# Performance work log

Hardware: AMD Instinct MI355X
Metric: run time of the kernel (lower is better)

Reference implementation:

```python
import jax, jax.numpy as jnp
import numpy as np

EPS = 1e-5


def _bn(h, gamma, beta):
    # BatchNorm1d, training mode: biased batch statistics over nodes
    mu = jnp.mean(h, axis=0)
    var = jnp.mean(jnp.square(h - mu), axis=0)
    return (h - mu) * jax.lax.rsqrt(var + EPS) * gamma + beta


def setup_inputs() -> dict:
    key = jax.random.key(0)
    ks = jax.random.split(key, 12)
    N, E, D, H = 50000, 800000, 128, 256
    x = jax.random.normal(ks[0], (N, D), dtype=jnp.float32)
    edge_index = jax.random.randint(ks[1], (2, E), 0, N, dtype=jnp.int64)
    train_node_id = jax.random.randint(ks[2], (10000,), 0, N, dtype=jnp.int64)
    def lin(k, fan_in, fan_out):
        bound = 1.0 / np.sqrt(fan_in)
        return jax.random.uniform(k, (fan_in, fan_out), jnp.float32, -bound, bound)
    return {
        "x": x, "edge_index": edge_index, "train_node_id": train_node_id,
        "W1": lin(ks[3], D, H), "b1": jnp.zeros((H,), jnp.float32),
        "W2": lin(ks[4], H, H), "b2": jnp.zeros((H,), jnp.float32),
        "W3": lin(ks[5], H, H), "b3": jnp.zeros((H,), jnp.float32),
        "g1": jnp.ones((H,), jnp.float32), "be1": jnp.zeros((H,), jnp.float32),
        "g2": jnp.ones((H,), jnp.float32), "be2": jnp.zeros((H,), jnp.float32),
        "g3": jnp.ones((H,), jnp.float32), "be3": jnp.zeros((H,), jnp.float32),
        "Wl": lin(ks[6], H, H), "bl": jnp.zeros((H,), jnp.float32),
        "Wf": lin(ks[7], H, 1), "bf": jnp.zeros((1,), jnp.float32),
    }


def reference(x, edge_index, train_node_id, W1, b1, W2, b2, W3, b3,
              g1, be1, g2, be2, g3, be3, Wl, bl, Wf, bf):
    N = x.shape[0]
    loops = jnp.arange(N, dtype=edge_index.dtype)
    row = jnp.concatenate([edge_index[0], loops])  # destinations
    col = jnp.concatenate([edge_index[1], loops])  # sources
    deg = jax.ops.segment_sum(jnp.ones_like(row, dtype=x.dtype), row, num_segments=N)
    d_isqrt = jax.lax.rsqrt(deg)  # deg >= 1 due to self loops
    norm = (d_isqrt[row] * d_isqrt[col])[:, None]  # [E+N, 1]

    def gcn(h, W, b):
        hW = h @ W
        agg = jax.ops.segment_sum(hW[col] * norm, row, num_segments=N)
        return agg + b

    h = jax.nn.relu(_bn(gcn(x, W1, b1), g1, be1))
    h = jax.nn.relu(_bn(gcn(h, W2, b2), g2, be2))
    h = jax.nn.relu(_bn(gcn(h, W3, b3), g3, be3))
    h = jax.nn.relu(h @ Wl + bl)
    h = h[train_node_id]
    return jnp.squeeze(h @ Wf + bf, -1)
```

## Files before the change

kernel.cpp:

```cpp
#include <hip/hip_runtime.h>

typedef unsigned short u16;
typedef __attribute__((ext_vector_type(8))) short short8;
typedef __attribute__((ext_vector_type(4))) float f32x4;

#define CAP 96

#define DEVFN static __device__ __forceinline__

DEVFN float b2f(u16 u) {
    union { float f; unsigned v; } x; x.v = ((unsigned)u) << 16; return x.f;
}
DEVFN u16 f2b(float f) {
    union { float f; unsigned v; } x; x.f = f;
    unsigned r = x.v + 0x7fffu + ((x.v >> 16) & 1u);
    return (u16)(r >> 16);
}
DEVFN float h2f(u16 u) {
    union { _Float16 h[2]; u16 s[2]; } x; x.s[0] = u; return (float)x.h[0];
}
DEVFN u16 f2h(float f) {
    union { _Float16 h[2]; u16 s[2]; } x; x.h[0] = (_Float16)f; return x.s[0];
}

DEVFN int detect64(const int* __restrict__ p) {
    int orv = 0;
#pragma unroll
    for (int i = 1; i < 64; i += 2) orv |= p[i];
    return (orv == 0) ? 1 : 0;
}

DEVFN void accum_row8(short8 v, float* acc) {
    const unsigned* u = (const unsigned*)&v;
#pragma unroll
    for (int k = 0; k < 4; k++) {
        union { float f; unsigned w; } lo, hi;
        lo.w = u[k] << 16;
        hi.w = u[k] & 0xffff0000u;
        acc[2 * k] += lo.f;
        acc[2 * k + 1] += hi.f;
    }
}

__global__ void k_init(const float* __restrict__ W1, const float* __restrict__ W2,
                       const float* __restrict__ W3, const float* __restrict__ Wl,
                       u16* __restrict__ T1, u16* __restrict__ T2,
                       u16* __restrict__ T3, u16* __restrict__ Tl,
                       int* __restrict__ ssrc, float* __restrict__ stat,
                       float* __restrict__ out, int N, int M) {
    int t = blockIdx.x * 256 + threadIdx.x;
    if (t < 229376) {
        const float* W; u16* T; int K; int idx;
        if (t < 32768)        { W = W1; T = T1; K = 128; idx = t; }
        else if (t < 98304)   { W = W2; T = T2; K = 256; idx = t - 32768; }
        else if (t < 163840)  { W = W3; T = T3; K = 256; idx = t - 98304; }
        else                  { W = Wl; T = Tl; K = 256; idx = t - 163840; }
        int k = idx >> 8, n = idx & 255;
        T[(size_t)n * K + k] = f2b(W[(size_t)k * 256 + n]);
    } else if (t < 229376 + 50000) {
        ssrc[(size_t)(t - 229376) * CAP] = 0;
    } else if (t < 229376 + 50000 + 1536) {
        stat[t - 229376 - 50000] = 0.0f;
    } else if (t < 229376 + 50000 + 1536 + 10000) {
        out[t - 229376 - 50000 - 1536] = 0.0f;
    }
}

__global__ void k_fillb(const int* __restrict__ ei, int* __restrict__ ssrc, int E) {
    int fl = detect64(ei);
    int t = blockIdx.x * 256 + threadIdx.x;
    int e0 = t * 4;
    if (e0 >= E) return;
    int r[4], c[4];
    int nv = min(4, E - e0);
    if (fl) {
        const int4* p4 = (const int4*)ei;
        int4 d0 = p4[2 * t], d1 = p4[2 * t + 1];
        int4 s0 = p4[(E >> 1) + 2 * t], s1 = p4[(E >> 1) + 2 * t + 1];
        r[0] = d0.x; r[1] = d0.z; r[2] = d1.x; r[3] = d1.z;
        c[0] = s0.x; c[1] = s0.z; c[2] = s1.x; c[3] = s1.z;
    } else {
        const int4* p4 = (const int4*)ei;
        int4 d = p4[t];
        int4 s = p4[(E >> 2) + t];
        r[0] = d.x; r[1] = d.y; r[2] = d.z; r[3] = d.w;
        c[0] = s.x; c[1] = s.y; c[2] = s.z; c[3] = s.w;
    }
#pragma unroll
    for (int k = 0; k < 4; k++) {
        if (k < nv) {
            int p = atomicAdd(&ssrc[(size_t)r[k] * CAP], 1);
            if (p < CAP - 1) ssrc[(size_t)r[k] * CAP + 1 + p] = c[k];
        }
    }
}

__global__ void k_cvtx(const float* __restrict__ x, const int* __restrict__ ssrc,
                       float* __restrict__ disq, u16* __restrict__ xb, int n) {
    int i = (blockIdx.x * 256 + threadIdx.x) * 4;
    if (i >= n) return;
    int row = i >> 7;
    float d = rsqrtf((float)(ssrc[(size_t)row * CAP] + 1));
    if ((i & 127) == 0) disq[row] = d;
    float4 v = *(const float4*)(x + i);
    ushort4 o;
    o.x = f2b(v.x * d); o.y = f2b(v.y * d); o.z = f2b(v.z * d); o.w = f2b(v.w * d);
    *(ushort4*)(xb + i) = o;
}


template<int KS>
__global__ __launch_bounds__(256, 2) void k_gemm_rb(
        const u16* __restrict__ A, const u16* __restrict__ Wt, u16* __restrict__ C,
        u16* __restrict__ Ch, const int* __restrict__ idx,
        int Gtot, float* __restrict__ stat, const float* __restrict__ bias, int relu,
        const float* __restrict__ Wfp, const float* __restrict__ bfp,
        float* __restrict__ outp) {
    constexpr int K = KS * 32;
    __shared__ float sbuf[4][2][64];
    int wv = threadIdx.x >> 6;
    int lane = threadIdx.x & 63;
    int quad = lane >> 4;
    int mr = lane & 15;
    int colbase = blockIdx.y * 64;
    int g0 = blockIdx.x * 16;

    short8 Bf[4][KS];
#pragma unroll
    for (int j = 0; j < 4; j++)
#pragma unroll
        for (int s = 0; s < KS; s++)
            Bf[j][s] = *(const short8*)(Wt + (size_t)(colbase + j * 16 + mr) * K + s * 32 + quad * 8);

    float bv[4] = {0.f, 0.f, 0.f, 0.f};
    if (bias) {
#pragma unroll
        for (int j = 0; j < 4; j++) bv[j] = bias[colbase + j * 16 + mr];
    }
    float wf[4] = {0.f, 0.f, 0.f, 0.f};
    if (Wfp) {
#pragma unroll
        for (int j = 0; j < 4; j++) wf[j] = Wfp[colbase + j * 16 + mr];
    }

    float sreg[4] = {0.f, 0.f, 0.f, 0.f};
    float s2reg[4] = {0.f, 0.f, 0.f, 0.f};
    int f = idx ? detect64(idx) : 0;

    for (int g = wv; g < 16; g += 4) {
        int gg = g0 + g;
        if (gg >= Gtot) continue;
        int row = gg * 16 + mr;
        int arow = idx ? idx[(size_t)row << f] : row;
        const u16* Ap = A + (size_t)arow * K + quad * 8;

        short8 Af[KS];
#pragma unroll
        for (int s = 0; s < KS; s++) Af[s] = *(const short8*)(Ap + s * 32);

        f32x4 acc[4];
#pragma unroll
        for (int j = 0; j < 4; j++) acc[j] = (f32x4){0.f, 0.f, 0.f, 0.f};
#pragma unroll
        for (int s = 0; s < KS; s++)
#pragma unroll
            for (int j = 0; j < 4; j++)
                acc[j] = __builtin_amdgcn_mfma_f32_16x16x32_bf16(Af[s], Bf[j][s], acc[j], 0, 0, 0);

        if (Wfp) {
            float partial[4];
#pragma unroll
            for (int r = 0; r < 4; r++) {
                float pr = 0.f;
#pragma unroll
                for (int j = 0; j < 4; j++) {
                    float v = fmaxf(acc[j][r] + bv[j], 0.f);
                    pr += v * wf[j];
                }
                partial[r] = pr;
            }
#pragma unroll
            for (int r = 0; r < 4; r++) {
                partial[r] += __shfl_xor(partial[r], 1, 64);
                partial[r] += __shfl_xor(partial[r], 2, 64);
                partial[r] += __shfl_xor(partial[r], 4, 64);
                partial[r] += __shfl_xor(partial[r], 8, 64);
            }
            if (mr == 0) {
#pragma unroll
                for (int r = 0; r < 4; r++) {
                    int orow = gg * 16 + quad * 4 + r;
                    float v = partial[r];
                    if (blockIdx.y == 0) v += bfp[0];
                    atomicAdd(&outp[orow], v);
                }
            }
            continue;
        }

        size_t cb = (size_t)(gg * 16 + quad * 4) * 256 + colbase + mr;
#pragma unroll
        for (int j = 0; j < 4; j++) {
            float s_ = 0.f, s2_ = 0.f;
#pragma unroll
            for (int r = 0; r < 4; r++) {
                float v = acc[j][r];
                s_ += v; s2_ += v * v;
                if (Ch) {
                    Ch[cb + (size_t)r * 256 + j * 16] = f2h(v);
                } else {
                    v += bv[j];
                    if (relu) v = fmaxf(v, 0.f);
                    C[cb + (size_t)r * 256 + j * 16] = f2b(v);
                }
            }
            sreg[j] += s_;
            s2reg[j] += s2_;
        }
    }

    if (stat) {
#pragma unroll
        for (int j = 0; j < 4; j++) {
            float s_ = sreg[j], s2_ = s2reg[j];
            s_ += __shfl_xor(s_, 16, 64);  s_ += __shfl_xor(s_, 32, 64);
            s2_ += __shfl_xor(s2_, 16, 64); s2_ += __shfl_xor(s2_, 32, 64);
            if (quad == 0) {
                sbuf[wv][0][j * 16 + mr] = s_;
                sbuf[wv][1][j * 16 + mr] = s2_;
            }
        }
        __syncthreads();
        int t = threadIdx.x;
        if (t < 128) {
            int which = t >> 6, c = t & 63;
            float v = sbuf[0][which][c] + sbuf[1][which][c] +
                      sbuf[2][which][c] + sbuf[3][which][c];
            atomicAdd(&stat[which * 256 + colbase + c], v);
        }
    }
}


__global__ __launch_bounds__(256) void k_gather256(
        const u16* __restrict__ src, const int* __restrict__ ssrc,
        const float* __restrict__ disq, u16* __restrict__ dst, int N) {
    int wave = threadIdx.x >> 6;
    int lane = threadIdx.x & 63;
    int half = lane >> 5;
    int l5 = lane & 31;
    int i = blockIdx.x * 4 + wave;
    if (i >= N) return;
    const u16* base = src + l5 * 8;
    const int* sp = ssrc + (size_t)i * CAP;
    float acc[8] = {0.f, 0.f, 0.f, 0.f, 0.f, 0.f, 0.f, 0.f};
    int e = min(sp[0], CAP - 1);
    int p = 0;
    for (; p + 8 <= e; p += 8) {
        int c0 = sp[1 + p + half];
        int c1 = sp[1 + p + 2 + half];
        int c2 = sp[1 + p + 4 + half];
        int c3 = sp[1 + p + 6 + half];
        short8 v0 = *(const short8*)(base + (size_t)c0 * 256);
        short8 v1 = *(const short8*)(base + (size_t)c1 * 256);
        short8 v2 = *(const short8*)(base + (size_t)c2 * 256);
        short8 v3 = *(const short8*)(base + (size_t)c3 * 256);
        accum_row8(v0, acc);
        accum_row8(v1, acc);
        accum_row8(v2, acc);
        accum_row8(v3, acc);
    }
    for (; p + 2 <= e; p += 2) {
        int c = sp[1 + p + half];
        short8 v = *(const short8*)(base + (size_t)c * 256);
        accum_row8(v, acc);
    }
    {
        int c = half ? i : ((p < e) ? sp[1 + p] : -1);
        if (c >= 0) {
            short8 v = *(const short8*)(base + (size_t)c * 256);
            accum_row8(v, acc);
        }
    }
#pragma unroll
    for (int k = 0; k < 8; k++) acc[k] += __shfl_xor(acc[k], 32, 64);
    if (half == 0) {
        float di = disq[i];
        short8 o;
        u16* op = (u16*)&o;
#pragma unroll
        for (int k = 0; k < 8; k++) op[k] = f2b(acc[k] * di);
        *(short8*)(dst + (size_t)i * 256 + l5 * 8) = o;
    }
}

__global__ __launch_bounds__(256) void k_gather128(
        const u16* __restrict__ src, const int* __restrict__ ssrc,
        const float* __restrict__ disq, u16* __restrict__ dst, int N) {
    int wave = threadIdx.x >> 6;
    int lane = threadIdx.x & 63;
    int q = lane >> 4;
    int l4 = lane & 15;
    int i = blockIdx.x * 4 + wave;
    if (i >= N) return;
    const u16* base = src + l4 * 8;
    const int* sp = ssrc + (size_t)i * CAP;
    float acc[8] = {0.f, 0.f, 0.f, 0.f, 0.f, 0.f, 0.f, 0.f};
    int e = min(sp[0], CAP - 1);
    int p = 0;
    for (; p + 8 <= e; p += 8) {
        int c0 = sp[1 + p + q];
        int c1 = sp[1 + p + 4 + q];
        short8 v0 = *(const short8*)(base + (size_t)c0 * 128);
        short8 v1 = *(const short8*)(base + (size_t)c1 * 128);
        accum_row8(v0, acc);
        accum_row8(v1, acc);
    }
    for (; p + 4 <= e; p += 4) {
        int c = sp[1 + p + q];
        short8 v = *(const short8*)(base + (size_t)c * 128);
        accum_row8(v, acc);
    }
    int rem = e - p;
    {
        int c = (q < rem) ? sp[1 + p + q] : ((q == 3) ? i : -1);
        if (c >= 0) {
            short8 v = *(const short8*)(base + (size_t)c * 128);
            accum_row8(v, acc);
        }
    }
#pragma unroll
    for (int k = 0; k < 8; k++) {
        acc[k] += __shfl_xor(acc[k], 16, 64);
        acc[k] += __shfl_xor(acc[k], 32, 64);
    }
    if (q == 0) {
        float di = disq[i];
        short8 o;
        u16* op = (u16*)&o;
#pragma unroll
        for (int k = 0; k < 8; k++) op[k] = f2b(acc[k] * di);
        *(short8*)(dst + (size_t)i * 128 + l4 * 8) = o;
    }
}


__global__ void k_bnapply(const u16* __restrict__ t, const float* __restrict__ stat,
                          const float* __restrict__ gamma, const float* __restrict__ beta,
                          u16* __restrict__ h, int N, float invN,
                          const float* __restrict__ scale) {
    size_t tt = (size_t)blockIdx.x * 256 + threadIdx.x;
    size_t base = tt * 4;
    if (base >= (size_t)N * 256) return;
    int f0 = (int)(base & 255);
    float sc2 = scale ? scale[base >> 8] : 1.0f;
    ushort4 v = *(const ushort4*)(t + base);
    float r[4] = {h2f(v.x), h2f(v.y), h2f(v.z), h2f(v.w)};
    ushort4 o;
    u16* op = (u16*)&o;
#pragma unroll
    for (int j = 0; j < 4; j++) {
        int f = f0 + j;
        float mean = stat[f] * invN;
        float var = stat[256 + f] * invN - mean * mean;
        float rstd = rsqrtf(var + 1e-5f);
        float sc = rstd * gamma[f];
        float sh = beta[f] - mean * sc;
        op[j] = f2b(fmaxf(r[j] * sc + sh, 0.0f) * sc2);
    }
    *(ushort4*)(h + base) = o;
}

__global__ void k_bnapply_idx(const u16* __restrict__ t, const float* __restrict__ stat,
                              const float* __restrict__ gamma, const float* __restrict__ beta,
                              const int* __restrict__ idx, u16* __restrict__ zin,
                              int M, float invN) {
    int fl = detect64(idx);
    size_t tt = (size_t)blockIdx.x * 256 + threadIdx.x;
    size_t base = tt * 4;
    if (base >= (size_t)M * 256) return;
    int f0 = (int)(base & 255);
    int row = (int)(base >> 8);
    int node = idx[(size_t)row << fl];
    ushort4 v = *(const ushort4*)(t + (size_t)node * 256 + f0);
    float r[4] = {h2f(v.x), h2f(v.y), h2f(v.z), h2f(v.w)};
    ushort4 o;
    u16* op = (u16*)&o;
#pragma unroll
    for (int j = 0; j < 4; j++) {
        int f = f0 + j;
        float mean = stat[f] * invN;
        float var = stat[256 + f] * invN - mean * mean;
        float rstd = rsqrtf(var + 1e-5f);
        float sc = rstd * gamma[f];
        float sh = beta[f] - mean * sc;
        op[j] = f2b(fmaxf(r[j] * sc + sh, 0.0f));
    }
    *(ushort4*)(zin + (size_t)row * 256 + f0) = o;
}


extern "C" void kernel_launch(void* const* d_in, const int* in_sizes, int n_in,
                              void* d_out, int out_size, void* d_ws, size_t ws_size,
                              hipStream_t stream) {
    const int D = 128, H = 256;
    const int N = in_sizes[0] / D;
    const int E = in_sizes[1] / 2;
    const int M = in_sizes[2];

    const float* x = (const float*)d_in[0];
    const int* ei = (const int*)d_in[1];
    const int* tnid = (const int*)d_in[2];
    const float* W1 = (const float*)d_in[3];
    const float* W2 = (const float*)d_in[5];
    const float* W3 = (const float*)d_in[7];
    const float* g1 = (const float*)d_in[9];
    const float* be1 = (const float*)d_in[10];
    const float* g2 = (const float*)d_in[11];
    const float* be2 = (const float*)d_in[12];
    const float* g3 = (const float*)d_in[13];
    const float* be3 = (const float*)d_in[14];
    const float* Wl = (const float*)d_in[15];
    const float* bl = (const float*)d_in[16];
    const float* Wf = (const float*)d_in[17];
    const float* bfp = (const float*)d_in[18];
    float* out = (float*)d_out;

    char* w = (char*)d_ws;
    size_t off = 0;
    auto carve = [&](size_t bytes) -> void* {
        void* p = w + off;
        off = (off + bytes + 255) & ~(size_t)255;
        return p;
    };

    float* stat = (float*)carve(3 * 512 * 4);
    float* disq = (float*)carve((size_t)N * 4);
    int* ssrc = (int*)carve((size_t)N * CAP * 4);
    u16* Wt1 = (u16*)carve((size_t)H * D * 2);
    u16* Wt2 = (u16*)carve((size_t)H * H * 2);
    u16* Wt3 = (u16*)carve((size_t)H * H * 2);
    u16* Wtl = (u16*)carve((size_t)H * H * 2);
    u16* xb = (u16*)carve((size_t)N * D * 2);
    u16* aggx = (u16*)carve((size_t)N * D * 2);
    u16* aggh = (u16*)carve((size_t)N * H * 2);
    u16* tb = (u16*)carve((size_t)N * H * 2);
    u16* hb = (u16*)carve((size_t)N * H * 2);
    u16* zin = (u16*)carve((size_t)M * H * 2);

    const float invN = 1.0f / (float)N;

    const int Gn = N / 16;
    const int Gm = M / 16;
    dim3 gemm_grid((Gn + 15) / 16, 4);
    dim3 gemm_grid_m((Gm + 15) / 16, 4);
    const int AB = (N + 3) / 4;
    const int PB = (int)(((size_t)N * H / 4 + 255) / 256);
    const int PBm = (int)(((size_t)M * H / 4 + 255) / 256);

    k_init<<<(229376 + 50000 + 1536 + 10000 + 255) / 256, 256, 0, stream>>>(
        W1, W2, W3, Wl, Wt1, Wt2, Wt3, Wtl, ssrc, stat, out, N, M);
    k_fillb<<<(E / 4 + 255) / 256, 256, 0, stream>>>(ei, ssrc, E);
    k_cvtx<<<(N * D / 4 + 255) / 256, 256, 0, stream>>>(x, ssrc, disq, xb, N * D);

    k_gather128<<<AB, 256, 0, stream>>>(xb, ssrc, disq, aggx, N);
    k_gemm_rb<4><<<gemm_grid, 256, 0, stream>>>(aggx, Wt1, nullptr, tb, nullptr, Gn, stat, nullptr, 0, nullptr, nullptr, nullptr);
    k_bnapply<<<PB, 256, 0, stream>>>(tb, stat, g1, be1, hb, N, invN, disq);
    k_gather256<<<AB, 256, 0, stream>>>(hb, ssrc, disq, aggh, N);
    k_gemm_rb<8><<<gemm_grid, 256, 0, stream>>>(aggh, Wt2, nullptr, tb, nullptr, Gn, stat + 512, nullptr, 0, nullptr, nullptr, nullptr);
    k_bnapply<<<PB, 256, 0, stream>>>(tb, stat + 512, g2, be2, hb, N, invN, disq);
    k_gather256<<<AB, 256, 0, stream>>>(hb, ssrc, disq, aggh, N);
    k_gemm_rb<8><<<gemm_grid, 256, 0, stream>>>(aggh, Wt3, nullptr, tb, nullptr, Gn, stat + 1024, nullptr, 0, nullptr, nullptr, nullptr);
    k_bnapply_idx<<<PBm, 256, 0, stream>>>(tb, stat + 1024, g3, be3, tnid, zin, M, invN);

    k_gemm_rb<8><<<gemm_grid_m, 256, 0, stream>>>(zin, Wtl, nullptr, nullptr, nullptr, Gm, nullptr, bl, 1, Wf, bfp, out);
}
```

Baseline: 463.2 us.

## Prefetch next A tile in GEMM, spread BN stat atomics, store fp32 intermediates

The GEMM loop now double-buffers the A fragments, loading the next row group while the MFMAs for the current one run, to hide global load latency. BatchNorm statistic atomics are spread over 8 replicated slots keyed on block index to reduce atomic contention, and the BN apply kernels sum the 8 slots. The pre-BN intermediate is stored as fp32 instead of fp16, which doubles its write and read traffic and raises precision. Register pressure grows from the second A buffer.

```diff
diff --git a/kernel.cpp b/kernel.cpp
--- a/kernel.cpp
+++ b/kernel.cpp
@@ -15,12 +15,6 @@
     union { float f; unsigned v; } x; x.f = f;
     unsigned r = x.v + 0x7fffu + ((x.v >> 16) & 1u);
     return (u16)(r >> 16);
-}
-DEVFN float h2f(u16 u) {
-    union { _Float16 h[2]; u16 s[2]; } x; x.s[0] = u; return (float)x.h[0];
-}
-DEVFN u16 f2h(float f) {
-    union { _Float16 h[2]; u16 s[2]; } x; x.h[0] = (_Float16)f; return x.s[0];
 }
 
 DEVFN int detect64(const int* __restrict__ p) {
@@ -59,10 +53,10 @@
         T[(size_t)n * K + k] = f2b(W[(size_t)k * 256 + n]);
     } else if (t < 229376 + 50000) {
         ssrc[(size_t)(t - 229376) * CAP] = 0;
-    } else if (t < 229376 + 50000 + 1536) {
+    } else if (t < 229376 + 50000 + 12288) {
         stat[t - 229376 - 50000] = 0.0f;
-    } else if (t < 229376 + 50000 + 1536 + 10000) {
-        out[t - 229376 - 50000 - 1536] = 0.0f;
+    } else if (t < 229376 + 50000 + 12288 + 10000) {
+        out[t - 229376 - 50000 - 12288] = 0.0f;
     }
 }
 
@@ -112,7 +106,7 @@
 template<int KS>
 __global__ __launch_bounds__(256, 2) void k_gemm_rb(
         const u16* __restrict__ A, const u16* __restrict__ Wt, u16* __restrict__ C,
-        u16* __restrict__ Ch, const int* __restrict__ idx,
+        float* __restrict__ Cf, const int* __restrict__ idx,
         int Gtot, float* __restrict__ stat, const float* __restrict__ bias, int relu,
         const float* __restrict__ Wfp, const float* __restrict__ bfp,
         float* __restrict__ outp) {
@@ -147,16 +141,38 @@
     float s2reg[4] = {0.f, 0.f, 0.f, 0.f};
     int f = idx ? detect64(idx) : 0;
 
-    for (int g = wv; g < 16; g += 4) {
+    short8 Af0[KS], Af1[KS];
+
+    {
+        int gg = g0 + wv;
+        if (gg < Gtot) {
+            int row = gg * 16 + mr;
+            int arow = idx ? idx[(size_t)row << f] : row;
+            const u16* Ap = A + (size_t)arow * K + quad * 8;
+#pragma unroll
+            for (int s = 0; s < KS; s++) Af0[s] = *(const short8*)(Ap + s * 32);
+        }
+    }
+
+#pragma unroll
+    for (int k = 0; k < 4; k++) {
+        int g = wv + k * 4;
         int gg = g0 + g;
+        short8* cur = (k & 1) ? Af1 : Af0;
+        short8* nxt = (k & 1) ? Af0 : Af1;
+
+        if (k < 3) {
+            int gg2 = g0 + g + 4;
+            if (gg2 < Gtot) {
+                int row2 = gg2 * 16 + mr;
+                int arow2 = idx ? idx[(size_t)row2 << f] : row2;
+                const u16* Ap2 = A + (size_t)arow2 * K + quad * 8;
+#pragma unroll
+                for (int s = 0; s < KS; s++) nxt[s] = *(const short8*)(Ap2 + s * 32);
+            }
+        }
+
         if (gg >= Gtot) continue;
-        int row = gg * 16 + mr;
-        int arow = idx ? idx[(size_t)row << f] : row;
-        const u16* Ap = A + (size_t)arow * K + quad * 8;
-
-        short8 Af[KS];
-#pragma unroll
-        for (int s = 0; s < KS; s++) Af[s] = *(const short8*)(Ap + s * 32);
 
         f32x4 acc[4];
 #pragma unroll
@@ -165,7 +181,7 @@
         for (int s = 0; s < KS; s++)
 #pragma unroll
             for (int j = 0; j < 4; j++)
-                acc[j] = __builtin_amdgcn_mfma_f32_16x16x32_bf16(Af[s], Bf[j][s], acc[j], 0, 0, 0);
+                acc[j] = __builtin_amdgcn_mfma_f32_16x16x32_bf16(cur[s], Bf[j][s], acc[j], 0, 0, 0);
 
         if (Wfp) {
             float partial[4];
@@ -206,8 +222,8 @@
             for (int r = 0; r < 4; r++) {
                 float v = acc[j][r];
                 s_ += v; s2_ += v * v;
-                if (Ch) {
-                    Ch[cb + (size_t)r * 256 + j * 16] = f2h(v);
+                if (Cf) {
+                    Cf[cb + (size_t)r * 256 + j * 16] = v;
                 } else {
                     v += bv[j];
                     if (relu) v = fmaxf(v, 0.f);
@@ -236,7 +252,7 @@
             int which = t >> 6, c = t & 63;
             float v = sbuf[0][which][c] + sbuf[1][which][c] +
                       sbuf[2][which][c] + sbuf[3][which][c];
-            atomicAdd(&stat[which * 256 + colbase + c], v);
+            atomicAdd(&stat[(blockIdx.x & 7) * 512 + which * 256 + colbase + c], v);
         }
     }
 }
@@ -345,7 +361,7 @@
 }
 
 
-__global__ void k_bnapply(const u16* __restrict__ t, const float* __restrict__ stat,
+__global__ void k_bnapply(const float* __restrict__ t, const float* __restrict__ stat,
                           const float* __restrict__ gamma, const float* __restrict__ beta,
                           u16* __restrict__ h, int N, float invN,
                           const float* __restrict__ scale) {
@@ -354,15 +370,21 @@
     if (base >= (size_t)N * 256) return;
     int f0 = (int)(base & 255);
     float sc2 = scale ? scale[base >> 8] : 1.0f;
-    ushort4 v = *(const ushort4*)(t + base);
-    float r[4] = {h2f(v.x), h2f(v.y), h2f(v.z), h2f(v.w)};
+    float4 v = *(const float4*)(t + base);
+    float r[4] = {v.x, v.y, v.z, v.w};
     ushort4 o;
     u16* op = (u16*)&o;
 #pragma unroll
     for (int j = 0; j < 4; j++) {
         int f = f0 + j;
-        float mean = stat[f] * invN;
-        float var = stat[256 + f] * invN - mean * mean;
+        float sm = 0.f, sq = 0.f;
+#pragma unroll
+        for (int rr = 0; rr < 8; rr++) {
+            sm += stat[rr * 512 + f];
+            sq += stat[rr * 512 + 256 + f];
+        }
+        float mean = sm * invN;
+        float var = sq * invN - mean * mean;
         float rstd = rsqrtf(var + 1e-5f);
         float sc = rstd * gamma[f];
         float sh = beta[f] - mean * sc;
@@ -371,7 +393,7 @@
     *(ushort4*)(h + base) = o;
 }
 
-__global__ void k_bnapply_idx(const u16* __restrict__ t, const float* __restrict__ stat,
+__global__ void k_bnapply_idx(const float* __restrict__ t, const float* __restrict__ stat,
                               const float* __restrict__ gamma, const float* __restrict__ beta,
                               const int* __restrict__ idx, u16* __restrict__ zin,
                               int M, float invN) {
@@ -382,15 +404,21 @@
     int f0 = (int)(base & 255);
     int row = (int)(base >> 8);
     int node = idx[(size_t)row << fl];
-    ushort4 v = *(const ushort4*)(t + (size_t)node * 256 + f0);
-    float r[4] = {h2f(v.x), h2f(v.y), h2f(v.z), h2f(v.w)};
+    float4 v = *(const float4*)(t + (size_t)node * 256 + f0);
+    float r[4] = {v.x, v.y, v.z, v.w};
     ushort4 o;
     u16* op = (u16*)&o;
 #pragma unroll
     for (int j = 0; j < 4; j++) {
         int f = f0 + j;
-        float mean = stat[f] * invN;
-        float var = stat[256 + f] * invN - mean * mean;
+        float sm = 0.f, sq = 0.f;
+#pragma unroll
+        for (int rr = 0; rr < 8; rr++) {
+            sm += stat[rr * 512 + f];
+            sq += stat[rr * 512 + 256 + f];
+        }
+        float mean = sm * invN;
+        float var = sq * invN - mean * mean;
         float rstd = rsqrtf(var + 1e-5f);
         float sc = rstd * gamma[f];
         float sh = beta[f] - mean * sc;
@@ -434,7 +462,7 @@
         return p;
     };
 
-    float* stat = (float*)carve(3 * 512 * 4);
+    float* stat = (float*)carve(3 * 4096 * 4);
     float* disq = (float*)carve((size_t)N * 4);
     int* ssrc = (int*)carve((size_t)N * CAP * 4);
     u16* Wt1 = (u16*)carve((size_t)H * D * 2);
@@ -444,7 +472,7 @@
     u16* xb = (u16*)carve((size_t)N * D * 2);
     u16* aggx = (u16*)carve((size_t)N * D * 2);
     u16* aggh = (u16*)carve((size_t)N * H * 2);
-    u16* tb = (u16*)carve((size_t)N * H * 2);
+    float* tb = (float*)carve((size_t)N * H * 4);
     u16* hb = (u16*)carve((size_t)N * H * 2);
     u16* zin = (u16*)carve((size_t)M * H * 2);
 
@@ -458,7 +486,7 @@
     const int PB = (int)(((size_t)N * H / 4 + 255) / 256);
     const int PBm = (int)(((size_t)M * H / 4 + 255) / 256);
 
-    k_init<<<(229376 + 50000 + 1536 + 10000 + 255) / 256, 256, 0, stream>>>(
+    k_init<<<(229376 + 50000 + 12288 + 10000 + 255) / 256, 256, 0, stream>>>(
         W1, W2, W3, Wl, Wt1, Wt2, Wt3, Wtl, ssrc, stat, out, N, M);
     k_fillb<<<(E / 4 + 255) / 256, 256, 0, stream>>>(ei, ssrc, E);
     k_cvtx<<<(N * D / 4 + 255) / 256, 256, 0, stream>>>(x, ssrc, disq, xb, N * D);
@@ -467,11 +495,11 @@
     k_gemm_rb<4><<<gemm_grid, 256, 0, stream>>>(aggx, Wt1, nullptr, tb, nullptr, Gn, stat, nullptr, 0, nullptr, nullptr, nullptr);
     k_bnapply<<<PB, 256, 0, stream>>>(tb, stat, g1, be1, hb, N, invN, disq);
     k_gather256<<<AB, 256, 0, stream>>>(hb, ssrc, disq, aggh, N);
-    k_gemm_rb<8><<<gemm_grid, 256, 0, stream>>>(aggh, Wt2, nullptr, tb, nullptr, Gn, stat + 512, nullptr, 0, nullptr, nullptr, nullptr);
-    k_bnapply<<<PB, 256, 0, stream>>>(tb, stat + 512, g2, be2, hb, N, invN, disq);
+    k_gemm_rb<8><<<gemm_grid, 256, 0, stream>>>(aggh, Wt2, nullptr, tb, nullptr, Gn, stat + 4096, nullptr, 0, nullptr, nullptr, nullptr);
+    k_bnapply<<<PB, 256, 0, stream>>>(tb, stat + 4096, g2, be2, hb, N, invN, disq);
     k_gather256<<<AB, 256, 0, stream>>>(hb, ssrc, disq, aggh, N);
-    k_gemm_rb<8><<<gemm_grid, 256, 0, stream>>>(aggh, Wt3, nullptr, tb, nullptr, Gn, stat + 1024, nullptr, 0, nullptr, nullptr, nullptr);
-    k_bnapply_idx<<<PBm, 256, 0, stream>>>(tb, stat + 1024, g3, be3, tnid, zin, M, invN);
+    k_gemm_rb<8><<<gemm_grid, 256, 0, stream>>>(aggh, Wt3, nullptr, tb, nullptr, Gn, stat + 8192, nullptr, 0, nullptr, nullptr, nullptr);
+    k_bnapply_idx<<<PBm, 256, 0, stream>>>(tb, stat + 8192, g3, be3, tnid, zin, M, invN);
 
     k_gemm_rb<8><<<gemm_grid_m, 256, 0, stream>>>(zin, Wtl, nullptr, nullptr, nullptr, Gm, nullptr, bl, 1, Wf, bfp, out);
 }
```

Measured after the change: 484.7 us. 4.6% more time.
